# Kernel optimization log

Hardware: AMD Instinct MI355X
Metric: run time of the kernel (lower is better)

Reference implementation:

```python
import jax, jax.numpy as jnp
import numpy as np

N_NODES = 50000
N_EDGES = 800000
D_IN = 128
D_HID = 128
D_OUT = 128


def _gcn_layer(x, W, b, src, dst, norm):
    # dense projection then edge-weighted gather -> scatter-add at dst
    h = x @ W                                   # [N, d_out]
    msg = h[src] * norm[:, None]                # [E, d_out]
    out = jax.ops.segment_sum(msg, dst, num_segments=N_NODES)
    return out + b


def setup_inputs() -> dict:
    key = jax.random.key(0)
    k = jax.random.split(key, 8)
    x = jax.random.normal(k[0], (N_NODES, D_IN), dtype=jnp.float32)
    edge_index = jax.random.randint(k[1], (2, N_EDGES), 0, N_NODES, dtype=jnp.int64)
    edge_weight = jax.random.uniform(k[2], (N_EDGES,), dtype=jnp.float32)
    # GCNConv params (glorot-ish scale)
    s1 = 1.0 / np.sqrt(D_IN)
    s2 = 1.0 / np.sqrt(D_HID)
    W1 = jax.random.normal(k[3], (D_IN, D_HID), dtype=jnp.float32) * s1
    b1 = jnp.zeros((D_HID,), dtype=jnp.float32)
    W2 = jax.random.normal(k[4], (D_HID, D_OUT), dtype=jnp.float32) * s2
    b2 = jnp.zeros((D_OUT,), dtype=jnp.float32)
    return {"x": x, "edge_index": edge_index, "edge_weight": edge_weight,
            "W1": W1, "b1": b1, "W2": W2, "b2": b2}


def reference(x, edge_index, edge_weight, W1, b1, W2, b2):
    src, dst = edge_index[0], edge_index[1]
    # gcn_norm (add_self_loops=False): deg from scatter-add of edge_weight at dst
    deg = jax.ops.segment_sum(edge_weight, dst, num_segments=N_NODES)
    dinv = jnp.where(deg > 0, jax.lax.rsqrt(jnp.maximum(deg, 1e-30)), 0.0)
    norm = dinv[src] * edge_weight * dinv[dst]  # [E]
    h = jax.nn.relu(_gcn_layer(x, W1, b1, src, dst, norm))
    out = _gcn_layer(h, W2, b2, src, dst, norm)
    # F.dropout in eval mode (deterministic reference) is identity
    return out
```

## Files before the change

kernel.cpp:

```cpp
#include <hip/hip_runtime.h>

#define N_NODES 50000
#define N_EDGES 800000
#define D 128
#define MAXDEG 64
#define NBUCK 196
#define BUCKCAP 5120
#define EPB 4096
#define NBB 196
#define SP 136

typedef __attribute__((ext_vector_type(8))) short bf16x8;
typedef __attribute__((ext_vector_type(4))) float f32x4;

__device__ inline unsigned short f2bf(float f) {
    unsigned u = __float_as_uint(f);
    unsigned r = (u + 0x7fffu + ((u >> 16) & 1u)) >> 16;
    return (unsigned short)r;
}

__global__ __launch_bounds__(256) void k_bucket(const int* __restrict__ src,
                                                const int* __restrict__ dst,
                                                const float* __restrict__ ew,
                                                int* __restrict__ cursor,
                                                uint2* __restrict__ buck,
                                                const float* __restrict__ W1,
                                                const float* __restrict__ W2,
                                                unsigned short* __restrict__ Wt1,
                                                unsigned short* __restrict__ Wt2) {
    if (blockIdx.x >= NBB) {
        const float* W = (blockIdx.x == NBB) ? W1 : W2;
        unsigned short* Wt = (blockIdx.x == NBB) ? Wt1 : Wt2;
        for (int idx = threadIdx.x; idx < D * D; idx += 256) {
            int n = idx & 127, k = idx >> 7;
            Wt[n * D + k] = f2bf(W[k * D + n]);
        }
        return;
    }
    __shared__ uint2 sorted[EPB];
    __shared__ int hist[NBUCK];
    __shared__ int scn[NBUCK];
    __shared__ int gbase[NBUCK];
    __shared__ int s[256];
    int tid = threadIdx.x;
    int e0 = blockIdx.x * EPB;
    for (int i = tid; i < NBUCK; i += 256) hist[i] = 0;
    __syncthreads();
    #pragma unroll
    for (int j = 0; j < 16; ++j) {
        int e = e0 + j * 256 + tid;
        if (e < N_EDGES) atomicAdd(&hist[dst[e] >> 8], 1);
    }
    __syncthreads();
    int v = tid < NBUCK ? hist[tid] : 0;
    s[tid] = v;
    __syncthreads();
    for (int off = 1; off < 256; off <<= 1) {
        int u = tid >= off ? s[tid - off] : 0;
        __syncthreads();
        s[tid] += u;
        __syncthreads();
    }
    int excl = s[tid] - v;
    if (tid < NBUCK) {
        scn[tid] = excl;
        gbase[tid] = v ? atomicAdd(&cursor[tid], v) : 0;
        hist[tid] = excl;
    }
    __syncthreads();
    #pragma unroll
    for (int j = 0; j < 16; ++j) {
        int e = e0 + j * 256 + tid;
        if (e < N_EDGES) {
            int d = dst[e];
            int sv = src[e];
            unsigned wf = min(__float2uint_rn(ew[e] * 65536.f), 65535u);
            int slot = atomicAdd(&hist[d >> 8], 1);
            sorted[slot] = make_uint2(((unsigned)sv << 16) | wf, (unsigned)d);
        }
    }
    __syncthreads();
    int total = min(EPB, N_EDGES - e0);
    for (int i = tid; i < total; i += 256) {
        uint2 en = sorted[i];
        int bk = (int)(en.y >> 8);
        int g = gbase[bk] + (i - scn[bk]);
        if (g < BUCKCAP)
            buck[(size_t)bk * BUCKCAP + g] = make_uint2(en.x, en.y & 255u);
    }
}

__global__ __launch_bounds__(256) void k_build(const int* __restrict__ cursor,
                                               const uint2* __restrict__ buck,
                                               unsigned* __restrict__ csr,
                                               int* __restrict__ cnt,
                                               float* __restrict__ dinv) {
    __shared__ unsigned csr_loc[256 * MAXDEG];
    __shared__ int cnt_loc[256];
    __shared__ int deg_loc[256];
    int b = blockIdx.x, tid = threadIdx.x;
    cnt_loc[tid] = 0;
    deg_loc[tid] = 0;
    __syncthreads();
    int n = min(cursor[b], BUCKCAP);
    const uint2* bb = buck + (size_t)b * BUCKCAP;
    for (int i = tid; i < n; i += 256) {
        uint2 e = bb[i];
        int ln = e.y;
        int slot = atomicAdd(&cnt_loc[ln], 1);
        if (slot < MAXDEG) csr_loc[ln * MAXDEG + slot] = e.x;
        atomicAdd(&deg_loc[ln], (int)(e.x & 0xffffu));
    }
    __syncthreads();
    int node0 = b * 256;
    int nnodes = min(256, N_NODES - node0);
    uint4* g = (uint4*)(csr + (size_t)node0 * MAXDEG);
    const uint4* l = (const uint4*)csr_loc;
    int nv = nnodes * (MAXDEG / 4);
    for (int i = tid; i < nv; i += 256) g[i] = l[i];
    if (tid < nnodes) {
        int node = node0 + tid;
        cnt[node] = min(cnt_loc[tid], MAXDEG);
        float sum = (float)deg_loc[tid] * (1.f / 65536.f);
        dinv[node] = sum > 0.f ? rsqrtf(fmaxf(sum, 1e-30f)) : 0.f;
    }
}

__global__ __launch_bounds__(256) void k_gemm(const float* __restrict__ X,
                                              const unsigned short* __restrict__ Wt,
                                              const float* __restrict__ dinv,
                                              unsigned short* __restrict__ Yb) {
    __shared__ unsigned short sX[64 * D];
    int row0 = blockIdx.x * 64;
    int nr = min(64, N_NODES - row0);
    {
        const float4* xs = (const float4*)(X + (size_t)row0 * D);
        int nvec = nr * (D / 4);
        for (int i = threadIdx.x; i < nvec; i += 256) {
            float4 v = xs[i];
            ushort4 o;
            o.x = f2bf(v.x); o.y = f2bf(v.y); o.z = f2bf(v.z); o.w = f2bf(v.w);
            *(ushort4*)(sX + i * 4) = o;
        }
    }
    __syncthreads();

    int wave = threadIdx.x >> 6, lane = threadIdx.x & 63;
    int m = lane & 15, quad = lane >> 4;
    f32x4 acc[8];
    #pragma unroll
    for (int i = 0; i < 8; ++i) acc[i] = (f32x4){0.f, 0.f, 0.f, 0.f};

    const unsigned short* aBase = sX + (wave * 16 + m) * D + quad * 8;
    #pragma unroll
    for (int c = 0; c < 4; ++c) {
        bf16x8 a = *(const bf16x8*)(aBase + c * 32);
        #pragma unroll
        for (int n0 = 0; n0 < 8; ++n0) {
            bf16x8 b = *(const bf16x8*)(Wt + (n0 * 16 + m) * D + c * 32 + quad * 8);
            acc[n0] = __builtin_amdgcn_mfma_f32_16x16x32_bf16(a, b, acc[n0], 0, 0, 0);
        }
    }

    float dv[4];
    #pragma unroll
    for (int i = 0; i < 4; ++i) {
        int r = row0 + wave * 16 + quad * 4 + i;
        dv[i] = r < N_NODES ? dinv[r] : 0.f;
    }

    unsigned short* sOut = sX + wave * 16 * D;
    __syncthreads();
    #pragma unroll
    for (int n0 = 0; n0 < 8; ++n0)
        #pragma unroll
        for (int i = 0; i < 4; ++i)
            sOut[(quad * 4 + i) * D + n0 * 16 + m] = f2bf(acc[n0][i] * dv[i]);
    __syncthreads();
    int rr = lane >> 2, c0 = (lane & 3) * 32;
    int grow = row0 + wave * 16 + rr;
    if (grow < N_NODES) {
        uint4* dstp = (uint4*)(Yb + (size_t)grow * D + c0);
        const uint4* srcp = (const uint4*)(sOut + rr * D + c0);
        dstp[0] = srcp[0]; dstp[1] = srcp[1]; dstp[2] = srcp[2]; dstp[3] = srcp[3];
    }
}

__global__ __launch_bounds__(256) void k_agg_mm(const unsigned short* __restrict__ H,
                                                const int* __restrict__ cnt,
                                                const unsigned* __restrict__ csr,
                                                const float* __restrict__ dinv,
                                                const float* __restrict__ b1,
                                                const unsigned short* __restrict__ Wt2,
                                                unsigned short* __restrict__ Hb) {
    __shared__ unsigned short sT[16 * SP];
    int tid = threadIdx.x, wave = tid >> 6, lane = tid & 63;
    int g = lane >> 4, fl = lane & 15;
    int nb = blockIdx.x * 16;

    for (int nn = 0; nn < 4; ++nn) {
        int node = nb + wave * 4 + nn;
        int end = min(cnt[node], MAXDEG);
        int nw = (end + 15) >> 4;
        const uint4* row4 = (const uint4*)(csr + (size_t)node * MAXDEG);
        uint4 c4[4];
        #pragma unroll
        for (int w = 0; w < 4; ++w)
            if (w < nw) c4[w] = row4[w * 4 + g];
        float acc[8] = {0.f, 0.f, 0.f, 0.f, 0.f, 0.f, 0.f, 0.f};
        #pragma unroll
        for (int w = 0; w < 4; ++w) {
            if (w < nw) {
                int k0 = w * 16 + g * 4;
                unsigned cs[4] = {c4[w].x, c4[w].y, c4[w].z, c4[w].w};
                #pragma unroll
                for (int j = 0; j < 4; ++j) {
                    if (k0 + j < end) {
                        unsigned sv = cs[j] >> 16;
                        float nm = (float)(cs[j] & 0xffffu) * (1.f / 65536.f);
                        uint4 u = *(const uint4*)(H + (size_t)sv * D + fl * 8);
                        unsigned a0[4] = {u.x, u.y, u.z, u.w};
                        #pragma unroll
                        for (int q = 0; q < 4; ++q) {
                            acc[2 * q]     += __uint_as_float(a0[q] << 16) * nm;
                            acc[2 * q + 1] += __uint_as_float(a0[q] & 0xffff0000u) * nm;
                        }
                    }
                }
            }
        }
        #pragma unroll
        for (int j = 0; j < 8; ++j) {
            acc[j] += __shfl_xor(acc[j], 16, 64);
            acc[j] += __shfl_xor(acc[j], 32, 64);
        }
        if (g < 2) {
            float dn = dinv[node];
            int f = fl * 8 + g * 4;
            ushort4 o;
            o.x = f2bf(fmaxf(acc[g * 4 + 0] * dn + b1[f + 0], 0.f));
            o.y = f2bf(fmaxf(acc[g * 4 + 1] * dn + b1[f + 1], 0.f));
            o.z = f2bf(fmaxf(acc[g * 4 + 2] * dn + b1[f + 2], 0.f));
            o.w = f2bf(fmaxf(acc[g * 4 + 3] * dn + b1[f + 3], 0.f));
            *(ushort4*)(sT + (wave * 4 + nn) * SP + f) = o;
        }
    }
    __syncthreads();

    int m = lane & 15, quad = lane >> 4;
    f32x4 acc2[2];
    acc2[0] = (f32x4){0.f, 0.f, 0.f, 0.f};
    acc2[1] = (f32x4){0.f, 0.f, 0.f, 0.f};
    #pragma unroll
    for (int c = 0; c < 4; ++c) {
        bf16x8 a = *(const bf16x8*)(sT + m * SP + c * 32 + quad * 8);
        #pragma unroll
        for (int t = 0; t < 2; ++t) {
            int n0 = wave * 2 + t;
            bf16x8 b = *(const bf16x8*)(Wt2 + (n0 * 16 + m) * D + c * 32 + quad * 8);
            acc2[t] = __builtin_amdgcn_mfma_f32_16x16x32_bf16(a, b, acc2[t], 0, 0, 0);
        }
    }
    float dv[4];
    #pragma unroll
    for (int i = 0; i < 4; ++i) dv[i] = dinv[nb + quad * 4 + i];
    __syncthreads();
    #pragma unroll
    for (int t = 0; t < 2; ++t)
        #pragma unroll
        for (int i = 0; i < 4; ++i)
            sT[(quad * 4 + i) * SP + (wave * 2 + t) * 16 + m] = f2bf(acc2[t][i] * dv[i]);
    __syncthreads();
    int rr = tid >> 4, cc = (tid & 15) * 8;
    *(uint4*)(Hb + (size_t)(nb + rr) * D + cc) = *(const uint4*)(sT + rr * SP + cc);
}

__global__ __launch_bounds__(256) void k_aggregate(const unsigned short* __restrict__ H,
                                                   const int* __restrict__ cnt,
                                                   const unsigned* __restrict__ csr,
                                                   const float* __restrict__ dinv,
                                                   const float* __restrict__ bias,
                                                   float* __restrict__ out) {
    int node = blockIdx.x * 4 + (threadIdx.x >> 6);
    int lane = threadIdx.x & 63;
    int g = lane >> 4;
    int fl = lane & 15;
    int end = min(cnt[node], MAXDEG);
    int nw = (end + 15) >> 4;
    const uint4* row4 = (const uint4*)(csr + (size_t)node * MAXDEG);
    uint4 c4[4];
    #pragma unroll
    for (int w = 0; w < 4; ++w)
        if (w < nw) c4[w] = row4[w * 4 + g];
    float acc[8] = {0.f, 0.f, 0.f, 0.f, 0.f, 0.f, 0.f, 0.f};
    #pragma unroll
    for (int w = 0; w < 4; ++w) {
        if (w < nw) {
            int k0 = w * 16 + g * 4;
            unsigned cs[4] = {c4[w].x, c4[w].y, c4[w].z, c4[w].w};
            #pragma unroll
            for (int j = 0; j < 4; ++j) {
                if (k0 + j < end) {
                    unsigned sv = cs[j] >> 16;
                    float nm = (float)(cs[j] & 0xffffu) * (1.f / 65536.f);
                    uint4 u = *(const uint4*)(H + (size_t)sv * D + fl * 8);
                    unsigned a0[4] = {u.x, u.y, u.z, u.w};
                    #pragma unroll
                    for (int q = 0; q < 4; ++q) {
                        acc[2 * q]     += __uint_as_float(a0[q] << 16) * nm;
                        acc[2 * q + 1] += __uint_as_float(a0[q] & 0xffff0000u) * nm;
                    }
                }
            }
        }
    }
    #pragma unroll
    for (int j = 0; j < 8; ++j) {
        acc[j] += __shfl_xor(acc[j], 16, 64);
        acc[j] += __shfl_xor(acc[j], 32, 64);
    }
    if (g < 2) {
        float dn = dinv[node];
        int f = fl * 8 + g * 4;
        *(float4*)(out + (size_t)node * D + f) =
            make_float4(acc[g * 4 + 0] * dn + bias[f + 0],
                        acc[g * 4 + 1] * dn + bias[f + 1],
                        acc[g * 4 + 2] * dn + bias[f + 2],
                        acc[g * 4 + 3] * dn + bias[f + 3]);
    }
}

extern "C" void kernel_launch(void* const* d_in, const int* in_sizes, int n_in,
                              void* d_out, int out_size, void* d_ws, size_t ws_size,
                              hipStream_t stream) {
    const float* x   = (const float*)d_in[0];
    const int*   ei  = (const int*)d_in[1];
    const float* ew  = (const float*)d_in[2];
    const float* W1  = (const float*)d_in[3];
    const float* b1  = (const float*)d_in[4];
    const float* W2  = (const float*)d_in[5];
    const float* b2  = (const float*)d_in[6];
    float* out = (float*)d_out;

    const int* src = ei;
    const int* dst = ei + N_EDGES;

    char* base = (char*)d_ws;
    size_t off = 0;
    auto take = [&](size_t bytes) -> char* {
        char* p = base + off;
        off += (bytes + 255) & ~(size_t)255;
        return p;
    };
    int*      cursor = (int*)take(NBUCK * 4);
    size_t zero_bytes = off;
    float*    dinv = (float*)take(N_NODES * 4);
    int*      cnt  = (int*)take(N_NODES * 4);
    uint2*    buck = (uint2*)take((size_t)NBUCK * BUCKCAP * 8);
    unsigned* csr  = (unsigned*)take((size_t)N_NODES * MAXDEG * 4);
    unsigned short* Wt1 = (unsigned short*)take(D * D * 2);
    unsigned short* Wt2 = (unsigned short*)take(D * D * 2);
    unsigned short* h0  = (unsigned short*)take((size_t)N_NODES * D * 2);
    unsigned short* hb  = (unsigned short*)take((size_t)N_NODES * D * 2);

    hipMemsetAsync(d_ws, 0, zero_bytes, stream);

    const int GB = (N_NODES + 63) / 64;
    const int FB = N_NODES / 16;
    const int AB = N_NODES / 4;

    k_bucket<<<NBB + 2, 256, 0, stream>>>(src, dst, ew, cursor, buck,
                                          W1, W2, Wt1, Wt2);
    k_build<<<NBUCK, 256, 0, stream>>>(cursor, buck, csr, cnt, dinv);

    k_gemm<<<GB, 256, 0, stream>>>(x, Wt1, dinv, h0);
    k_agg_mm<<<FB, 256, 0, stream>>>(h0, cnt, csr, dinv, b1, Wt2, hb);
    k_aggregate<<<AB, 256, 0, stream>>>(hb, cnt, csr, dinv, b2, out);
}
```

Before: 212.2 us.

## Merge CSR build and first GEMM into one launch, move dinv[src] scaling to aggregation

The CSR build and the layer-1 projection GEMM now run as one kernel with disjoint block ranges. This works because the GEMM no longer multiplies rows by dinv. The source-side dinv factor is instead applied per edge inside the first aggregation, which removes a launch and the dependency between the two stages. The cost is an extra random dinv[src] load per edge in k_agg_mm, a larger shared-memory union that may lower occupancy for GEMM blocks, and slightly different bf16 rounding.

```diff
diff --git a/kernel.cpp b/kernel.cpp
--- a/kernel.cpp
+++ b/kernel.cpp
@@ -90,97 +90,96 @@
     }
 }
 
-__global__ __launch_bounds__(256) void k_build(const int* __restrict__ cursor,
-                                               const uint2* __restrict__ buck,
-                                               unsigned* __restrict__ csr,
-                                               int* __restrict__ cnt,
-                                               float* __restrict__ dinv) {
-    __shared__ unsigned csr_loc[256 * MAXDEG];
-    __shared__ int cnt_loc[256];
-    __shared__ int deg_loc[256];
-    int b = blockIdx.x, tid = threadIdx.x;
-    cnt_loc[tid] = 0;
-    deg_loc[tid] = 0;
-    __syncthreads();
-    int n = min(cursor[b], BUCKCAP);
-    const uint2* bb = buck + (size_t)b * BUCKCAP;
-    for (int i = tid; i < n; i += 256) {
-        uint2 e = bb[i];
-        int ln = e.y;
-        int slot = atomicAdd(&cnt_loc[ln], 1);
-        if (slot < MAXDEG) csr_loc[ln * MAXDEG + slot] = e.x;
-        atomicAdd(&deg_loc[ln], (int)(e.x & 0xffffu));
-    }
-    __syncthreads();
-    int node0 = b * 256;
-    int nnodes = min(256, N_NODES - node0);
-    uint4* g = (uint4*)(csr + (size_t)node0 * MAXDEG);
-    const uint4* l = (const uint4*)csr_loc;
-    int nv = nnodes * (MAXDEG / 4);
-    for (int i = tid; i < nv; i += 256) g[i] = l[i];
-    if (tid < nnodes) {
-        int node = node0 + tid;
-        cnt[node] = min(cnt_loc[tid], MAXDEG);
-        float sum = (float)deg_loc[tid] * (1.f / 65536.f);
-        dinv[node] = sum > 0.f ? rsqrtf(fmaxf(sum, 1e-30f)) : 0.f;
-    }
-}
-
-__global__ __launch_bounds__(256) void k_gemm(const float* __restrict__ X,
-                                              const unsigned short* __restrict__ Wt,
-                                              const float* __restrict__ dinv,
-                                              unsigned short* __restrict__ Yb) {
-    __shared__ unsigned short sX[64 * D];
-    int row0 = blockIdx.x * 64;
+#define GB 782
+__global__ __launch_bounds__(256) void k_build_gemm(
+        const int* __restrict__ cursor, const uint2* __restrict__ buck,
+        unsigned* __restrict__ csr, int* __restrict__ cnt,
+        float* __restrict__ dinv,
+        const float* __restrict__ X, const unsigned short* __restrict__ Wt1,
+        unsigned short* __restrict__ h0) {
+    __shared__ union SM {
+        struct {
+            unsigned csr_loc[256 * MAXDEG];
+            int cnt_loc[256];
+            int deg_loc[256];
+        } b;
+        unsigned short sX[64 * D];
+    } sm;
+    int tid = threadIdx.x;
+
+    if (blockIdx.x < NBUCK) {
+        int b = blockIdx.x;
+        sm.b.cnt_loc[tid] = 0;
+        sm.b.deg_loc[tid] = 0;
+        __syncthreads();
+        int n = min(cursor[b], BUCKCAP);
+        const uint2* bb = buck + (size_t)b * BUCKCAP;
+        for (int i = tid; i < n; i += 256) {
+            uint2 e = bb[i];
+            int ln = e.y;
+            int slot = atomicAdd(&sm.b.cnt_loc[ln], 1);
+            if (slot < MAXDEG) sm.b.csr_loc[ln * MAXDEG + slot] = e.x;
+            atomicAdd(&sm.b.deg_loc[ln], (int)(e.x & 0xffffu));
+        }
+        __syncthreads();
+        int node0 = b * 256;
+        int nnodes = min(256, N_NODES - node0);
+        uint4* g = (uint4*)(csr + (size_t)node0 * MAXDEG);
+        const uint4* l = (const uint4*)sm.b.csr_loc;
+        int nv = nnodes * (MAXDEG / 4);
+        for (int i = tid; i < nv; i += 256) g[i] = l[i];
+        if (tid < nnodes) {
+            int node = node0 + tid;
+            cnt[node] = min(sm.b.cnt_loc[tid], MAXDEG);
+            float sum = (float)sm.b.deg_loc[tid] * (1.f / 65536.f);
+            dinv[node] = sum > 0.f ? rsqrtf(fmaxf(sum, 1e-30f)) : 0.f;
+        }
+        return;
+    }
+
+    int row0 = (blockIdx.x - NBUCK) * 64;
     int nr = min(64, N_NODES - row0);
     {
         const float4* xs = (const float4*)(X + (size_t)row0 * D);
         int nvec = nr * (D / 4);
-        for (int i = threadIdx.x; i < nvec; i += 256) {
+        for (int i = tid; i < nvec; i += 256) {
             float4 v = xs[i];
             ushort4 o;
             o.x = f2bf(v.x); o.y = f2bf(v.y); o.z = f2bf(v.z); o.w = f2bf(v.w);
-            *(ushort4*)(sX + i * 4) = o;
-        }
-    }
-    __syncthreads();
-
-    int wave = threadIdx.x >> 6, lane = threadIdx.x & 63;
+            *(ushort4*)(sm.sX + i * 4) = o;
+        }
+    }
+    __syncthreads();
+
+    int wave = tid >> 6, lane = tid & 63;
     int m = lane & 15, quad = lane >> 4;
     f32x4 acc[8];
     #pragma unroll
     for (int i = 0; i < 8; ++i) acc[i] = (f32x4){0.f, 0.f, 0.f, 0.f};
 
-    const unsigned short* aBase = sX + (wave * 16 + m) * D + quad * 8;
+    const unsigned short* aBase = sm.sX + (wave * 16 + m) * D + quad * 8;
     #pragma unroll
     for (int c = 0; c < 4; ++c) {
         bf16x8 a = *(const bf16x8*)(aBase + c * 32);
         #pragma unroll
         for (int n0 = 0; n0 < 8; ++n0) {
-            bf16x8 b = *(const bf16x8*)(Wt + (n0 * 16 + m) * D + c * 32 + quad * 8);
+            bf16x8 b = *(const bf16x8*)(Wt1 + (n0 * 16 + m) * D + c * 32 + quad * 8);
             acc[n0] = __builtin_amdgcn_mfma_f32_16x16x32_bf16(a, b, acc[n0], 0, 0, 0);
         }
     }
 
-    float dv[4];
-    #pragma unroll
-    for (int i = 0; i < 4; ++i) {
-        int r = row0 + wave * 16 + quad * 4 + i;
-        dv[i] = r < N_NODES ? dinv[r] : 0.f;
-    }
-
-    unsigned short* sOut = sX + wave * 16 * D;
+    unsigned short* sOut = sm.sX + wave * 16 * D;
     __syncthreads();
     #pragma unroll
     for (int n0 = 0; n0 < 8; ++n0)
         #pragma unroll
         for (int i = 0; i < 4; ++i)
-            sOut[(quad * 4 + i) * D + n0 * 16 + m] = f2bf(acc[n0][i] * dv[i]);
+            sOut[(quad * 4 + i) * D + n0 * 16 + m] = f2bf(acc[n0][i]);
     __syncthreads();
     int rr = lane >> 2, c0 = (lane & 3) * 32;
     int grow = row0 + wave * 16 + rr;
     if (grow < N_NODES) {
-        uint4* dstp = (uint4*)(Yb + (size_t)grow * D + c0);
+        uint4* dstp = (uint4*)(h0 + (size_t)grow * D + c0);
         const uint4* srcp = (const uint4*)(sOut + rr * D + c0);
         dstp[0] = srcp[0]; dstp[1] = srcp[1]; dstp[2] = srcp[2]; dstp[3] = srcp[3];
     }
@@ -217,7 +216,8 @@
                 for (int j = 0; j < 4; ++j) {
                     if (k0 + j < end) {
                         unsigned sv = cs[j] >> 16;
-                        float nm = (float)(cs[j] & 0xffffu) * (1.f / 65536.f);
+                        float nm = (float)(cs[j] & 0xffffu) * (1.f / 65536.f)
+                                   * dinv[sv];
                         uint4 u = *(const uint4*)(H + (size_t)sv * D + fl * 8);
                         unsigned a0[4] = {u.x, u.y, u.z, u.w};
                         #pragma unroll
@@ -365,15 +365,13 @@
 
     hipMemsetAsync(d_ws, 0, zero_bytes, stream);
 
-    const int GB = (N_NODES + 63) / 64;
     const int FB = N_NODES / 16;
     const int AB = N_NODES / 4;
 
     k_bucket<<<NBB + 2, 256, 0, stream>>>(src, dst, ew, cursor, buck,
                                           W1, W2, Wt1, Wt2);
-    k_build<<<NBUCK, 256, 0, stream>>>(cursor, buck, csr, cnt, dinv);
-
-    k_gemm<<<GB, 256, 0, stream>>>(x, Wt1, dinv, h0);
+    k_build_gemm<<<NBUCK + GB, 256, 0, stream>>>(cursor, buck, csr, cnt, dinv,
+                                                 x, Wt1, h0);
     k_agg_mm<<<FB, 256, 0, stream>>>(h0, cnt, csr, dinv, b1, Wt2, hb);
     k_aggregate<<<AB, 256, 0, stream>>>(hb, cnt, csr, dinv, b2, out);
 }
```

Result: faster. 204.3 us (median of 2 runs) (-3.7%).
